# Optimization experiments

Measured on AMD Instinct MI355X. Metric: run time of the kernel, lower is better.

Reference implementation:

```python
import jax, jax.numpy as jnp
import numpy as np

E = 256
H = 8
DK = E // H


def setup_inputs() -> dict:
    key = jax.random.key(0)
    ks = jax.random.split(key, 16)
    B, NA, NB = 2, 2048, 2048
    x_a = jax.random.normal(ks[0], (B, NA, E), dtype=jnp.float32)
    x_b = jax.random.normal(ks[1], (B, NB, E), dtype=jnp.float32)
    s = 1.0 / np.sqrt(E)  # kaiming-normal-ish scale
    inp = {"x_a": x_a, "x_b": x_b}
    names = ["wq", "wk_a", "wk_b", "wv_a", "wv_b", "w"]
    for i, n in enumerate(names):
        inp[n + "_w"] = jax.random.normal(ks[2 + 2 * i], (E, E), dtype=jnp.float32) * s
        inp[n + "_b"] = jax.random.normal(ks[3 + 2 * i], (E,), dtype=jnp.float32) * 0.01
    return inp


def _linear(x, w, b):
    # torch nn.Linear: y = x @ w.T + b
    return jnp.einsum('bne,fe->bnf', x, w) + b


def _heads(x):
    # [B, N, E] -> [B, H, N, DK]
    B, N, _ = x.shape
    return x.reshape(B, N, H, DK).transpose(0, 2, 1, 3)


def reference(x_a, x_b, wq_w, wq_b, wk_a_w, wk_a_b, wk_b_w, wk_b_b,
              wv_a_w, wv_a_b, wv_b_w, wv_b_b, w_w, w_b):
    B, NA, _ = x_a.shape
    q = _heads(_linear(x_a, wq_w, wq_b))          # [B,H,NA,DK]
    k_a = _heads(_linear(x_a, wk_a_w, wk_a_b))    # [B,H,NA,DK]
    v_a = _heads(_linear(x_a, wv_a_w, wv_a_b))
    k_b = _heads(_linear(x_b, wk_b_w, wk_b_b))    # [B,H,NB,DK]
    v_b = _heads(_linear(x_b, wv_b_w, wv_b_b))
    k = jnp.concatenate([k_a, k_b], axis=2)       # [B,H,NA+NB,DK]
    v = jnp.concatenate([v_a, v_b], axis=2)
    scores = jnp.einsum('bhqd,bhkd->bhqk', q, k) / jnp.sqrt(jnp.float32(DK))
    p = jax.nn.softmax(scores, axis=-1)           # [B,H,NA,NA+NB]
    z = jnp.einsum('bhqk,bhkd->bhqd', p, v)       # [B,H,NA,DK]
    z = z.transpose(0, 2, 1, 3).reshape(B, NA, E)
    out = _linear(z, w_w, w_b) + x_a
    return out
```

## Files before the change

kernel.cpp:

```cpp
#include <hip/hip_runtime.h>
#include <cstdint>

typedef short bf16x8 __attribute__((ext_vector_type(8)));
typedef float f32x4 __attribute__((ext_vector_type(4)));
typedef unsigned short u16;
typedef unsigned int u32;

#define DEVI static __device__ __forceinline__


DEVI u16 f2bf(float f) {
  u32 x = __builtin_bit_cast(u32, f);
  x += 0x7fffu + ((x >> 16) & 1u);
  return (u16)(x >> 16);
}

DEVI u32 pack_bf2(float lo, float hi) {
  return (u32)f2bf(lo) | ((u32)f2bf(hi) << 16);
}

DEVI u32 cvt_pk_bf16(float lo, float hi) {
  u32 r;
  asm("v_cvt_pk_bf16_f32 %0, %1, %2" : "=v"(r) : "v"(lo), "v"(hi));
  return r;
}

DEVI f32x4 mfma16(bf16x8 a, bf16x8 b, f32x4 c) {
  return __builtin_amdgcn_mfma_f32_16x16x32_bf16(a, b, c, 0, 0, 0);
}

DEVI void load_lds16(const void* g, void* l) {
  __builtin_amdgcn_global_load_lds(
      (const __attribute__((address_space(1))) u32*)g,
      (__attribute__((address_space(3))) u32*)l, 16, 0, 0);
}

#define CSCALE 0.2550351f

DEVI int rho(int k) {
  return ((k >> 5) << 5) | (((k >> 2) & 1) << 4) | (((k >> 3) & 3) << 2) | (k & 3);
}

__global__ __launch_bounds__(256) void convert_kernel(
    const float* __restrict__ xa, const float* __restrict__ xb,
    const float* __restrict__ w0, const float* __restrict__ w1,
    const float* __restrict__ w2, const float* __restrict__ w3,
    const float* __restrict__ w4, const float* __restrict__ w5,
    u16* __restrict__ dst) {
  int i = (int)(blockIdx.x * 256u + threadIdx.x) * 8;
  const float* s;
  if (i < 1048576) {
    s = xa + i;
  } else if (i < 2097152) {
    s = xb + (i - 1048576);
  } else {
    int t = i - 2097152;
    int j = t >> 16, o = t & 65535;
    s = (j == 0 ? w0 : j == 1 ? w1 : j == 2 ? w2 : j == 3 ? w3 : j == 4 ? w4 : w5) + o;
  }
  float4 a = *(const float4*)s;
  float4 b = *(const float4*)(s + 4);
  uint4 o4;
  o4.x = pack_bf2(a.x, a.y);
  o4.y = pack_bf2(a.z, a.w);
  o4.z = pack_bf2(b.x, b.y);
  o4.w = pack_bf2(b.z, b.w);
  *(uint4*)(dst + i) = o4;
}

__global__ __launch_bounds__(256) void proj_kernel(
    const u16* __restrict__ xa_bf, const u16* __restrict__ xb_bf,
    const u16* __restrict__ wbase,
    const float* __restrict__ b0, const float* __restrict__ b1,
    const float* __restrict__ b2, const float* __restrict__ b3,
    const float* __restrict__ b4,
    u16* __restrict__ Qo, u16* __restrict__ Ko, u16* __restrict__ Vo) {
  int job = blockIdx.z;
  const u16* A = (job <= 2) ? xa_bf : xb_bf;
  const u16* W = wbase + job * 65536;
  const float* bias = job == 0 ? b0 : job == 1 ? b1 : job == 2 ? b2 : job == 3 ? b3 : b4;
  int mode = (job == 0) ? 0 : (job == 1 || job == 3) ? 1 : 2;
  int soff = (job >= 3) ? 2048 : 0;

  int tid = threadIdx.x, wid = tid >> 6, lane = tid & 63, g = lane >> 4, c = lane & 15;
  int m0 = blockIdx.x * 64, n0 = blockIdx.y * 64;
  const u16* Ap = A + (size_t)(m0 + wid * 16 + c) * 256 + g * 8;
  const u16* Wp = W + (n0 + c) * 256 + g * 8;
  f32x4 acc[4] = {};
#pragma unroll
  for (int kk = 0; kk < 256; kk += 32) {
    bf16x8 af = *(const bf16x8*)(Ap + kk);
#pragma unroll
    for (int nt = 0; nt < 4; ++nt) {
      bf16x8 bfr = *(const bf16x8*)(Wp + nt * 4096 + kk);
      acc[nt] = mfma16(af, bfr, acc[nt]);
    }
  }
#pragma unroll
  for (int nt = 0; nt < 4; ++nt) {
    int f = n0 + nt * 16 + c;
    float bv = bias[f];
    int h = f >> 5, d = f & 31;
#pragma unroll
    for (int r = 0; r < 4; ++r) {
      int m = m0 + wid * 16 + g * 4 + r;
      int bq = m >> 11, n = m & 2047;
      int bh = bq * 8 + h;
      float y = acc[nt][r] + bv;
      if (mode == 0) {
        Qo[((size_t)bh * 2048 + n) * 32 + d] = f2bf(y * CSCALE);
      } else if (mode == 1) {
        int nk = soff + n;
        int pr = (nk & ~63) | rho(nk & 63);
        Ko[((size_t)bh * 4096 + pr) * 32 + d] = f2bf(y);
      } else {
        int nk = soff + n;
        Vo[(size_t)bh * 131072 + (nk >> 6) * 2048 + ((nk >> 3) & 7) * 256 +
           d * 8 + (nk & 7)] = f2bf(y);
      }
    }
  }
}

__global__ __launch_bounds__(256) void attn_kernel(
    const u16* __restrict__ Q, const u16* __restrict__ K,
    const u16* __restrict__ Vt, float* __restrict__ Zp, float* __restrict__ S) {
  __shared__ __align__(16) unsigned char sbuf[24576];
  int bid = blockIdx.x;
  int xcd = bid & 7, slot = bid >> 3;
  int bh = (xcd << 1) | (slot & 1);
  int rem = slot >> 1;
  int ks = rem & 3, qi = rem >> 2;
  int tid = threadIdx.x, wid = tid >> 6, lane = tid & 63;
  int g = lane >> 4, c = lane & 15;
  int qbase = qi * 64 + wid * 16;

  const unsigned char* Kb =
      (const unsigned char*)K + (size_t)bh * 262144 + (size_t)ks * 65536;
  const unsigned char* Vb =
      (const unsigned char*)Vt + (size_t)bh * 262144 + (size_t)ks * 65536;

  bf16x8 qf = *(const bf16x8*)(Q + ((size_t)bh * 2048 + qbase + c) * 32 + g * 8);

  int kaddr = c * 64 + ((g ^ ((c >> 1) & 3)) << 4);
  int vaddr = g * 512 + c * 16;

  int o = wid * 1024 + (lane << 4);
  int ko_src = o ^ (((o >> 7) & 3) << 4);

  f32x4 z0 = {}, z1 = {};
  float lsum = 0.f;

  load_lds16(Kb + ko_src, sbuf + wid * 1024);
  load_lds16(Vb + o, sbuf + 12288 + wid * 1024);

  int cur = 0;
  for (int t = 0; t < 16; ++t) {
    int nxt = cur + 1;
    if (nxt == 3) nxt = 0;
    if (t + 1 < 16) {
      load_lds16(Kb + (t + 1) * 4096 + ko_src, sbuf + nxt * 4096 + wid * 1024);
      load_lds16(Vb + (t + 1) * 4096 + o, sbuf + 12288 + nxt * 4096 + wid * 1024);
      __builtin_amdgcn_sched_barrier(0);
      asm volatile("s_waitcnt vmcnt(2)" ::: "memory");
    } else {
      __builtin_amdgcn_sched_barrier(0);
      asm volatile("s_waitcnt vmcnt(0)" ::: "memory");
    }
    __builtin_amdgcn_s_barrier();
    __builtin_amdgcn_sched_barrier(0);

    const unsigned char* kbuf = sbuf + cur * 4096;
    const unsigned char* vbuf = sbuf + 12288 + cur * 4096;

    bf16x8 kf0 = *(const bf16x8*)(kbuf + kaddr);
    bf16x8 kf1 = *(const bf16x8*)(kbuf + kaddr + 1024);
    bf16x8 kf2 = *(const bf16x8*)(kbuf + kaddr + 2048);
    bf16x8 kf3 = *(const bf16x8*)(kbuf + kaddr + 3072);
    bf16x8 vf00 = *(const bf16x8*)(vbuf + vaddr);
    bf16x8 vf01 = *(const bf16x8*)(vbuf + vaddr + 2048);
    bf16x8 vf10 = *(const bf16x8*)(vbuf + vaddr + 256);
    bf16x8 vf11 = *(const bf16x8*)(vbuf + vaddr + 2048 + 256);

    f32x4 zz = {};
    __builtin_amdgcn_s_setprio(1);
    f32x4 s0 = mfma16(kf0, qf, zz);
    f32x4 s1 = mfma16(kf1, qf, zz);
    f32x4 s2 = mfma16(kf2, qf, zz);
    f32x4 s3 = mfma16(kf3, qf, zz);
    __builtin_amdgcn_s_setprio(0);

    float e0[4], e1[4], e2[4], e3[4];
#pragma unroll
    for (int r = 0; r < 4; ++r) {
      e0[r] = __builtin_amdgcn_exp2f(s0[r]);
      e1[r] = __builtin_amdgcn_exp2f(s1[r]);
      e2[r] = __builtin_amdgcn_exp2f(s2[r]);
      e3[r] = __builtin_amdgcn_exp2f(s3[r]);
    }
    lsum += ((e0[0] + e0[1]) + (e0[2] + e0[3])) + ((e1[0] + e1[1]) + (e1[2] + e1[3])) +
            ((e2[0] + e2[1]) + (e2[2] + e2[3])) + ((e3[0] + e3[1]) + (e3[2] + e3[3]));

    union { u32 u[4]; bf16x8 v; } A0, A1;
    A0.u[0] = cvt_pk_bf16(e0[0], e0[1]);
    A0.u[1] = cvt_pk_bf16(e0[2], e0[3]);
    A0.u[2] = cvt_pk_bf16(e1[0], e1[1]);
    A0.u[3] = cvt_pk_bf16(e1[2], e1[3]);
    A1.u[0] = cvt_pk_bf16(e2[0], e2[1]);
    A1.u[1] = cvt_pk_bf16(e2[2], e2[3]);
    A1.u[2] = cvt_pk_bf16(e3[0], e3[1]);
    A1.u[3] = cvt_pk_bf16(e3[2], e3[3]);

    __builtin_amdgcn_s_setprio(1);
    z0 = mfma16(A0.v, vf00, z0);
    z0 = mfma16(A1.v, vf01, z0);
    z1 = mfma16(A0.v, vf10, z1);
    z1 = mfma16(A1.v, vf11, z1);
    __builtin_amdgcn_s_setprio(0);
    cur = nxt;
  }

  lsum += __shfl_xor(lsum, 16);
  lsum += __shfl_xor(lsum, 32);

  size_t zrow = ((size_t)ks * 16 + bh) * 2048;
  if (lane < 16) S[zrow + qbase + lane] = lsum;
#pragma unroll
  for (int r = 0; r < 4; ++r) {
    int m = qbase + g * 4 + r;
    float* zp = Zp + (zrow + m) * 32;
    zp[c] = z0[r];
    zp[16 + c] = z1[r];
  }
}

__global__ __launch_bounds__(256) void out_kernel(
    const float* __restrict__ Zp, const float* __restrict__ S,
    const u16* __restrict__ W, const float* __restrict__ bias,
    const float* __restrict__ resid, float* __restrict__ out) {
  int tid = threadIdx.x, wid = tid >> 6, lane = tid & 63, g = lane >> 4, c = lane & 15;
  int m0 = blockIdx.x * 16;
  int mrow = m0 + c;
  int bq = mrow >> 11, n = mrow & 2047;
  const u16* Wp = W + (size_t)(wid * 64 + c) * 256 + g * 8;

  f32x4 acc[4] = {};
#pragma unroll
  for (int h = 0; h < 8; ++h) {
    int bh = bq * 8 + h;
    size_t sb = (size_t)bh * 2048 + n;
    float ts = (S[sb] + S[sb + 32768]) + (S[sb + 65536] + S[sb + 98304]);
    float iv = 1.0f / ts;
    const float* zp = Zp + sb * 32 + g * 8;
    float4 a0 = *(const float4*)zp;
    float4 a1 = *(const float4*)(zp + 4);
    float4 b0 = *(const float4*)(zp + 1048576);
    float4 b1 = *(const float4*)(zp + 1048576 + 4);
    float4 c0 = *(const float4*)(zp + 2097152);
    float4 c1 = *(const float4*)(zp + 2097152 + 4);
    float4 d0 = *(const float4*)(zp + 3145728);
    float4 d1 = *(const float4*)(zp + 3145728 + 4);
    float e0 = ((a0.x + b0.x) + (c0.x + d0.x)) * iv;
    float e1 = ((a0.y + b0.y) + (c0.y + d0.y)) * iv;
    float e2 = ((a0.z + b0.z) + (c0.z + d0.z)) * iv;
    float e3 = ((a0.w + b0.w) + (c0.w + d0.w)) * iv;
    float e4 = ((a1.x + b1.x) + (c1.x + d1.x)) * iv;
    float e5 = ((a1.y + b1.y) + (c1.y + d1.y)) * iv;
    float e6 = ((a1.z + b1.z) + (c1.z + d1.z)) * iv;
    float e7 = ((a1.w + b1.w) + (c1.w + d1.w)) * iv;
    union { u32 u[4]; bf16x8 v; } af;
    af.u[0] = cvt_pk_bf16(e0, e1);
    af.u[1] = cvt_pk_bf16(e2, e3);
    af.u[2] = cvt_pk_bf16(e4, e5);
    af.u[3] = cvt_pk_bf16(e6, e7);
#pragma unroll
    for (int nt = 0; nt < 4; ++nt) {
      bf16x8 bfr = *(const bf16x8*)(Wp + nt * 4096 + h * 32);
      acc[nt] = mfma16(af.v, bfr, acc[nt]);
    }
  }
#pragma unroll
  for (int nt = 0; nt < 4; ++nt) {
    int f = wid * 64 + nt * 16 + c;
    float bv = bias[f];
#pragma unroll
    for (int r = 0; r < 4; ++r) {
      int m = m0 + g * 4 + r;
      out[(size_t)m * 256 + f] = acc[nt][r] + bv + resid[(size_t)m * 256 + f];
    }
  }
}

extern "C" void kernel_launch(void* const* d_in, const int* in_sizes, int n_in,
                              void* d_out, int out_size, void* d_ws, size_t ws_size,
                              hipStream_t stream) {
  const float* xa = (const float*)d_in[0];
  const float* xb = (const float*)d_in[1];
  const float* wq_w = (const float*)d_in[2];
  const float* wq_b = (const float*)d_in[3];
  const float* wka_w = (const float*)d_in[4];
  const float* wka_b = (const float*)d_in[5];
  const float* wkb_w = (const float*)d_in[6];
  const float* wkb_b = (const float*)d_in[7];
  const float* wva_w = (const float*)d_in[8];
  const float* wva_b = (const float*)d_in[9];
  const float* wvb_w = (const float*)d_in[10];
  const float* wvb_b = (const float*)d_in[11];
  const float* w_w = (const float*)d_in[12];
  const float* w_b = (const float*)d_in[13];

  u16* ws = (u16*)d_ws;
  u16* xa_bf = ws;
  u16* xb_bf = ws + 1048576;
  u16* wbf = ws + 2097152;
  u16* Qb = ws + 2490368;
  u16* Kb = ws + 3538944;
  u16* Vtb = ws + 5636096;
  float* Zp = (float*)(ws + 7733248);
  float* S = Zp + 4194304;

  convert_kernel<<<1216, 256, 0, stream>>>(xa, xb, wq_w, wka_w, wva_w, wkb_w,
                                           wvb_w, w_w, ws);
  proj_kernel<<<dim3(64, 4, 5), 256, 0, stream>>>(
      xa_bf, xb_bf, wbf, wq_b, wka_b, wva_b, wkb_b, wvb_b, Qb, Kb, Vtb);
  attn_kernel<<<2048, 256, 0, stream>>>(Qb, Kb, Vtb, Zp, S);
  out_kernel<<<256, 256, 0, stream>>>(Zp, S, wbf + 5 * 65536, w_b, xa,
                                      (float*)d_out);
}
```

Before: 80.68 us.

## Process four query fragments per wave to reuse K/V tiles, compute row sums via MFMA

```diff
diff --git a/kernel.cpp b/kernel.cpp
--- a/kernel.cpp
+++ b/kernel.cpp
@@ -133,14 +133,18 @@
   int ks = rem & 3, qi = rem >> 2;
   int tid = threadIdx.x, wid = tid >> 6, lane = tid & 63;
   int g = lane >> 4, c = lane & 15;
-  int qbase = qi * 64 + wid * 16;
+  int qbase = qi * 256 + wid * 64;
 
   const unsigned char* Kb =
       (const unsigned char*)K + (size_t)bh * 262144 + (size_t)ks * 65536;
   const unsigned char* Vb =
       (const unsigned char*)Vt + (size_t)bh * 262144 + (size_t)ks * 65536;
 
-  bf16x8 qf = *(const bf16x8*)(Q + ((size_t)bh * 2048 + qbase + c) * 32 + g * 8);
+  const u16* Qp = Q + ((size_t)bh * 2048 + qbase + c) * 32 + g * 8;
+  bf16x8 qf0 = *(const bf16x8*)(Qp);
+  bf16x8 qf1 = *(const bf16x8*)(Qp + 16 * 32);
+  bf16x8 qf2 = *(const bf16x8*)(Qp + 32 * 32);
+  bf16x8 qf3 = *(const bf16x8*)(Qp + 48 * 32);
 
   int kaddr = c * 64 + ((g ^ ((c >> 1) & 3)) << 4);
   int vaddr = g * 512 + c * 16;
@@ -148,8 +152,13 @@
   int o = wid * 1024 + (lane << 4);
   int ko_src = o ^ (((o >> 7) & 3) << 4);
 
-  f32x4 z0 = {}, z1 = {};
-  float lsum = 0.f;
+  const u32 one2 = 0x3F803F80u;
+  union { u32 u[4]; bf16x8 v; } ones;
+  ones.u[0] = one2; ones.u[1] = one2; ones.u[2] = one2; ones.u[3] = one2;
+
+  f32x4 z00 = {}, z01 = {}, z10 = {}, z11 = {};
+  f32x4 z20 = {}, z21 = {}, z30 = {}, z31 = {};
+  f32x4 zs0 = {}, zs1 = {}, zs2 = {}, zs3 = {};
 
   load_lds16(Kb + ko_src, sbuf + wid * 1024);
   load_lds16(Vb + o, sbuf + 12288 + wid * 1024);
@@ -182,56 +191,65 @@
     bf16x8 vf10 = *(const bf16x8*)(vbuf + vaddr + 256);
     bf16x8 vf11 = *(const bf16x8*)(vbuf + vaddr + 2048 + 256);
 
-    f32x4 zz = {};
-    __builtin_amdgcn_s_setprio(1);
-    f32x4 s0 = mfma16(kf0, qf, zz);
-    f32x4 s1 = mfma16(kf1, qf, zz);
-    f32x4 s2 = mfma16(kf2, qf, zz);
-    f32x4 s3 = mfma16(kf3, qf, zz);
-    __builtin_amdgcn_s_setprio(0);
-
-    float e0[4], e1[4], e2[4], e3[4];
-#pragma unroll
-    for (int r = 0; r < 4; ++r) {
-      e0[r] = __builtin_amdgcn_exp2f(s0[r]);
-      e1[r] = __builtin_amdgcn_exp2f(s1[r]);
-      e2[r] = __builtin_amdgcn_exp2f(s2[r]);
-      e3[r] = __builtin_amdgcn_exp2f(s3[r]);
-    }
-    lsum += ((e0[0] + e0[1]) + (e0[2] + e0[3])) + ((e1[0] + e1[1]) + (e1[2] + e1[3])) +
-            ((e2[0] + e2[1]) + (e2[2] + e2[3])) + ((e3[0] + e3[1]) + (e3[2] + e3[3]));
-
-    union { u32 u[4]; bf16x8 v; } A0, A1;
-    A0.u[0] = cvt_pk_bf16(e0[0], e0[1]);
-    A0.u[1] = cvt_pk_bf16(e0[2], e0[3]);
-    A0.u[2] = cvt_pk_bf16(e1[0], e1[1]);
-    A0.u[3] = cvt_pk_bf16(e1[2], e1[3]);
-    A1.u[0] = cvt_pk_bf16(e2[0], e2[1]);
-    A1.u[1] = cvt_pk_bf16(e2[2], e2[3]);
-    A1.u[2] = cvt_pk_bf16(e3[0], e3[1]);
-    A1.u[3] = cvt_pk_bf16(e3[2], e3[3]);
-
-    __builtin_amdgcn_s_setprio(1);
-    z0 = mfma16(A0.v, vf00, z0);
-    z0 = mfma16(A1.v, vf01, z0);
-    z1 = mfma16(A0.v, vf10, z1);
-    z1 = mfma16(A1.v, vf11, z1);
-    __builtin_amdgcn_s_setprio(0);
+#define QFRAG(QF, ZA, ZB, ZS)                                              \
+    {                                                                      \
+      f32x4 zz = {};                                                       \
+      __builtin_amdgcn_s_setprio(1);                                       \
+      f32x4 s0 = mfma16(kf0, QF, zz);                                      \
+      f32x4 s1 = mfma16(kf1, QF, zz);                                      \
+      f32x4 s2 = mfma16(kf2, QF, zz);                                      \
+      f32x4 s3 = mfma16(kf3, QF, zz);                                      \
+      __builtin_amdgcn_s_setprio(0);                                       \
+      float e0[4], e1[4], e2[4], e3[4];                                    \
+      _Pragma("unroll")                                                    \
+      for (int r = 0; r < 4; ++r) {                                        \
+        e0[r] = __builtin_amdgcn_exp2f(s0[r]);                             \
+        e1[r] = __builtin_amdgcn_exp2f(s1[r]);                             \
+        e2[r] = __builtin_amdgcn_exp2f(s2[r]);                             \
+        e3[r] = __builtin_amdgcn_exp2f(s3[r]);                             \
+      }                                                                    \
+      union { u32 u[4]; bf16x8 v; } A0, A1;                                \
+      A0.u[0] = cvt_pk_bf16(e0[0], e0[1]);                                 \
+      A0.u[1] = cvt_pk_bf16(e0[2], e0[3]);                                 \
+      A0.u[2] = cvt_pk_bf16(e1[0], e1[1]);                                 \
+      A0.u[3] = cvt_pk_bf16(e1[2], e1[3]);                                 \
+      A1.u[0] = cvt_pk_bf16(e2[0], e2[1]);                                 \
+      A1.u[1] = cvt_pk_bf16(e2[2], e2[3]);                                 \
+      A1.u[2] = cvt_pk_bf16(e3[0], e3[1]);                                 \
+      A1.u[3] = cvt_pk_bf16(e3[2], e3[3]);                                 \
+      __builtin_amdgcn_s_setprio(1);                                       \
+      ZA = mfma16(A0.v, vf00, ZA);                                         \
+      ZA = mfma16(A1.v, vf01, ZA);                                         \
+      ZB = mfma16(A0.v, vf10, ZB);                                         \
+      ZB = mfma16(A1.v, vf11, ZB);                                         \
+      ZS = mfma16(A0.v, ones.v, ZS);                                       \
+      ZS = mfma16(A1.v, ones.v, ZS);                                       \
+      __builtin_amdgcn_s_setprio(0);                                       \
+    }
+
+    QFRAG(qf0, z00, z01, zs0)
+    QFRAG(qf1, z10, z11, zs1)
+    QFRAG(qf2, z20, z21, zs2)
+    QFRAG(qf3, z30, z31, zs3)
+#undef QFRAG
     cur = nxt;
   }
 
-  lsum += __shfl_xor(lsum, 16);
-  lsum += __shfl_xor(lsum, 32);
-
   size_t zrow = ((size_t)ks * 16 + bh) * 2048;
-  if (lane < 16) S[zrow + qbase + lane] = lsum;
-#pragma unroll
-  for (int r = 0; r < 4; ++r) {
-    int m = qbase + g * 4 + r;
-    float* zp = Zp + (zrow + m) * 32;
-    zp[c] = z0[r];
-    zp[16 + c] = z1[r];
-  }
+#define STORE(J, ZA, ZB, ZS)                                               \
+  _Pragma("unroll")                                                        \
+  for (int r = 0; r < 4; ++r) {                                            \
+    int m = qbase + J * 16 + g * 4 + r;                                    \
+    float* zp = Zp + (zrow + m) * 32;                                      \
+    zp[c] = ZA[r];                                                         \
+    zp[16 + c] = ZB[r];                                                    \
+    if (c == 0) S[zrow + m] = ZS[r];                                       \
+  }
+  STORE(0, z00, z01, zs0)
+  STORE(1, z10, z11, zs1)
+  STORE(2, z20, z21, zs2)
+  STORE(3, z30, z31, zs3)
+#undef STORE
 }
 
 __global__ __launch_bounds__(256) void out_kernel(
@@ -323,7 +341,7 @@
                                            wvb_w, w_w, ws);
   proj_kernel<<<dim3(64, 4, 5), 256, 0, stream>>>(
       xa_bf, xb_bf, wbf, wq_b, wka_b, wva_b, wkb_b, wvb_b, Qb, Kb, Vtb);
-  attn_kernel<<<2048, 256, 0, stream>>>(Qb, Kb, Vtb, Zp, S);
+  attn_kernel<<<512, 256, 0, stream>>>(Qb, Kb, Vtb, Zp, S);
   out_kernel<<<256, 256, 0, stream>>>(Zp, S, wbf + 5 * 65536, w_b, xa,
                                       (float*)d_out);
 }
```

Result: no change. 79.49 us (-1.5%).
